# Kernel tuning notes

Measured on AMD Instinct MI355X. Metric: run time of the kernel, lower is better.

## Reference

```python
import jax, jax.numpy as jnp
import numpy as np
from jax import lax

B, T, D = 32, 1024, 512
UNITS, WINDOW = 512, 3


def setup_inputs() -> dict:
    key = jax.random.key(0)
    k1, k2 = jax.random.split(key)
    x = jax.random.normal(k1, (B, T, D), dtype=jnp.float32)
    kernel = jax.random.normal(k2, (WINDOW, D, UNITS * 3), dtype=jnp.float32) * 0.05
    return {"x": x, "kernel": kernel}


def reference(x, kernel):
    units = kernel.shape[2] // 3
    # valid conv1d, channels_last: [B, T, D] x [W, D, 3U] -> [B, T-W+1, 3U]
    conv = lax.conv_general_dilated(
        x, kernel, window_strides=(1,), padding='VALID',
        dimension_numbers=('NWC', 'WIO', 'NWC'))
    Z = conv[..., :units]
    F = conv[..., units:2 * units]
    O = conv[..., 2 * units:]
    z = jnp.tanh(Z)
    f = jax.nn.sigmoid(F)
    o = jax.nn.sigmoid(O)

    # fo-pooling recurrence over time (time-major scan)
    def step(c, zfo):
        z_t, f_t, o_t = zfo
        c_t = f_t * c + (1.0 - f_t) * z_t
        return c_t, o_t * c_t

    c0 = jnp.zeros((x.shape[0], units), dtype=x.dtype)
    zf = (z.transpose(1, 0, 2), f.transpose(1, 0, 2), o.transpose(1, 0, 2))
    _, hs = lax.scan(step, c0, zf)
    return hs.transpose(1, 0, 2)  # [B, T-W+1, units] (ret_sequence=True)
```

## Files before the change

kernel.cpp:

```cpp
#include <hip/hip_runtime.h>
#include <hip/hip_bf16.h>

typedef unsigned short u16;
typedef unsigned short u16x8 __attribute__((ext_vector_type(8)));
typedef short s16x8 __attribute__((ext_vector_type(8)));
typedef float f32x4 __attribute__((ext_vector_type(4)));

#define BATCH 32
#define TPAD 1024
#define TOUT 1022
#define DIM 512
#define KDIM 1536
#define NDIM 1536
#define MPAD (BATCH * TPAD)

#define XB_ELEMS  (MPAD * DIM + 1024)
#define XB_BYTES  (XB_ELEMS * 2)
#define WT_ELEMS  (NDIM * KDIM)
#define WT_BYTES  (WT_ELEMS * 2)
#define ACTS_OFF  (XB_BYTES + WT_BYTES)

__device__ __forceinline__ u16 f2bf(float f) {
    union { __hip_bfloat16 h; u16 u; } v;
    v.h = __float2bfloat16(f);
    return v.u;
}
__device__ __forceinline__ float bf2f(u16 u) {
    union { unsigned int i; float f; } v;
    v.i = ((unsigned int)u) << 16;
    return v.f;
}

__device__ __forceinline__ void gload_lds16(const void* g, void* l) {
    __builtin_amdgcn_global_load_lds(
        (const __attribute__((address_space(1))) void*)g,
        (__attribute__((address_space(3))) void*)l, 16, 0, 0);
}

#define BARRIER() do { asm volatile("" ::: "memory"); \
                       __builtin_amdgcn_s_barrier(); \
                       asm volatile("" ::: "memory"); } while (0)

__global__ __launch_bounds__(256) void cvt_x_kernel(const float* __restrict__ x,
                                                    u16* __restrict__ xb) {
    const int n = MPAD * DIM;
    const int ntot = XB_ELEMS;
    int i = (blockIdx.x * 256 + threadIdx.x) * 8;
    if (i >= ntot) return;
    if (i + 8 <= n) {
        const float4* p = (const float4*)(x + i);
        float4 a = p[0], b = p[1];
        u16x8 r;
        r[0] = f2bf(a.x); r[1] = f2bf(a.y); r[2] = f2bf(a.z); r[3] = f2bf(a.w);
        r[4] = f2bf(b.x); r[5] = f2bf(b.y); r[6] = f2bf(b.z); r[7] = f2bf(b.w);
        *(u16x8*)(xb + i) = r;
    } else {
        for (int q = 0; q < 8 && i + q < ntot; q++)
            xb[i + q] = (i + q < n) ? f2bf(x[i + q]) : (u16)0;
    }
}

__global__ __launch_bounds__(256) void cvt_w_kernel(const float* __restrict__ w,
                                                    u16* __restrict__ wT) {
    __shared__ u16 tile[32][33];
    int tx = threadIdx.x & 31, ty = threadIdx.x >> 5;
    int kt = blockIdx.x * 32, jt = blockIdx.y * 32;
#pragma unroll
    for (int q = 0; q < 4; q++) {
        int k = kt + ty + q * 8;
        tile[ty + q * 8][tx] = f2bf(w[(size_t)k * NDIM + jt + tx]);
    }
    __syncthreads();
#pragma unroll
    for (int q = 0; q < 4; q++) {
        int j = jt + ty + q * 8;
        wT[(size_t)j * KDIM + kt + tx] = tile[tx][ty + q * 8];
    }
}

__global__ __launch_bounds__(512, 2) void gemm_kernel(const u16* __restrict__ xb,
                                                      const u16* __restrict__ wT,
                                                      u16* __restrict__ acts) {
    __shared__ u16 lsA[256 * 64];
    __shared__ u16 lsB[256 * 64];

    const int tid  = threadIdx.x;
    const int lane = tid & 63;
    const int w    = tid >> 6;
    const int wr   = w >> 2;
    const int wc   = w & 3;

    const int wg  = blockIdx.x;
    const int gid = (wg & 7) * 96 + (wg >> 3);
    const int bm  = gid / 6;
    const int bn  = gid % 6;

    const int l15  = lane & 15;
    const int kgrp = (lane >> 4) * 16;
    const int xorv = (lane & 7) << 4;

    const int sc = ((lane & 7) ^ (lane >> 3)) << 4;
    const char* gsrc[8];
    char* ldst[8];
    {
        const char* gA = (const char*)xb;
        const char* gB = (const char*)wT;
#pragma unroll
        for (int g = 0; g < 4; g++) {
            int r0 = wr * 128 + g * 32 + wc * 8;
            int idx = (g < 2) ? g : (4 + g);
            gsrc[idx] = gA + (size_t)(bm * 256 + r0 + (lane >> 3)) * 1024 + sc;
            ldst[idx] = (char*)lsA + r0 * 128;
        }
#pragma unroll
        for (int h = 0; h < 4; h++) {
            int r0 = wc * 64 + h * 16 + wr * 8;
            int idx = 2 + h;
            gsrc[idx] = gB + (size_t)(bn * 256 + r0 + (lane >> 3)) * 3072 + sc;
            ldst[idx] = (char*)lsB + r0 * 128;
        }
    }

    f32x4 acc[8][4] = {};
    s16x8 a[4][2];
    s16x8 b[2][2][2];

#define STAGE(IDX) gload_lds16(gsrc[IDX] + koff, ldst[IDX])

#define LOAD_A(QM) \
    _Pragma("unroll") for (int ii = 0; ii < 4; ii++) \
    _Pragma("unroll") for (int kk = 0; kk < 2; kk++) { \
        int row = wr * 128 + (QM) * 64 + ii * 16 + l15; \
        int byte = (row * 128 + kk * 64 + kgrp) ^ xorv; \
        a[ii][kk] = *(const s16x8*)((const char*)lsA + byte); }

#define LOAD_B(QN) \
    _Pragma("unroll") for (int jj = 0; jj < 2; jj++) \
    _Pragma("unroll") for (int kk = 0; kk < 2; kk++) { \
        int row = wc * 64 + (QN) * 32 + jj * 16 + l15; \
        int byte = (row * 128 + kk * 64 + kgrp) ^ xorv; \
        b[QN][jj][kk] = *(const s16x8*)((const char*)lsB + byte); }

#define MFMA_QUAD(QM, QN) \
    __builtin_amdgcn_s_setprio(1); \
    _Pragma("unroll") for (int ii = 0; ii < 4; ii++) \
    _Pragma("unroll") for (int jj = 0; jj < 2; jj++) \
    _Pragma("unroll") for (int kk = 0; kk < 2; kk++) \
        acc[(QM)*4+ii][(QN)*2+jj] = __builtin_amdgcn_mfma_f32_16x16x32_bf16( \
            a[ii][kk], b[QN][jj][kk], acc[(QM)*4+ii][(QN)*2+jj], 0, 0, 0); \
    __builtin_amdgcn_s_setprio(0);

    {
        size_t koff = 0;
        STAGE(0); STAGE(1); STAGE(2); STAGE(3);
        STAGE(4); STAGE(5); STAGE(6); STAGE(7);
    }

    const int NT = KDIM / 64;
    for (int kt = 0; kt < NT; kt++) {
        const int knext = (kt + 1 == NT) ? 0 : (kt + 1);
        const size_t koff = (size_t)knext * 128;

        asm volatile("s_waitcnt vmcnt(4)" ::: "memory");
        BARRIER();
        LOAD_A(0)
        LOAD_B(0)
        MFMA_QUAD(0, 0)
        BARRIER();

        asm volatile("s_waitcnt vmcnt(2)" ::: "memory");
        BARRIER();
        STAGE(0); STAGE(1); STAGE(2); STAGE(3);
        LOAD_B(1)
        MFMA_QUAD(0, 1)
        BARRIER();

        asm volatile("s_waitcnt vmcnt(4)" ::: "memory");
        BARRIER();
        STAGE(4); STAGE(5);
        LOAD_A(1)
        MFMA_QUAD(1, 1)
        BARRIER();

        STAGE(6); STAGE(7);
        MFMA_QUAD(1, 0)
        BARRIER();
    }

    asm volatile("s_waitcnt vmcnt(0)" ::: "memory");

#undef STAGE
#undef LOAD_A
#undef LOAD_B
#undef MFMA_QUAD

    const int m0 = bm * 256 + wr * 128 + ((lane >> 4) << 2);
    const int n0 = bn * 256 + wc * 64 + (lane & 15);
#pragma unroll
    for (int i = 0; i < 8; i++)
#pragma unroll
        for (int j = 0; j < 4; j++)
#pragma unroll
            for (int r = 0; r < 4; r++) {
                int m = m0 + i * 16 + r;
                int n = n0 + j * 16;
                acts[(size_t)m * NDIM + n] = f2bf(acc[i][j][r]);
            }
}

#define CHUNK 64
__global__ __launch_bounds__(1024) void scan_kernel(const u16* __restrict__ acts,
                                                    float* __restrict__ out) {
    __shared__ float sA[16][64];
    __shared__ float sB[16][64];
    const int lane = threadIdx.x & 63;
    const int w = threadIdx.x >> 6;
    const int b = blockIdx.x >> 3;
    const int u = ((blockIdx.x & 7) << 6) + lane;
    const u16* base = acts + (size_t)b * TPAD * NDIM;
    const int t0 = w * CHUNK;
    const int t1 = (t0 + CHUNK < TOUT) ? (t0 + CHUNK) : TOUT;

    float A = 1.f, Bc = 0.f;
    int t = t0;
    for (; t + 8 <= t1; t += 8) {
        u16 zv[8], fv[8];
#pragma unroll
        for (int q = 0; q < 8; q++) {
            const u16* r = base + (size_t)(t + q) * NDIM;
            zv[q] = r[u]; fv[q] = r[512 + u];
        }
#pragma unroll
        for (int q = 0; q < 8; q++) {
            float z = tanhf(bf2f(zv[q]));
            float f = 1.f / (1.f + __expf(-bf2f(fv[q])));
            Bc = f * Bc + (1.f - f) * z;
            A *= f;
        }
    }
    for (; t < t1; t++) {
        const u16* r = base + (size_t)t * NDIM;
        float z = tanhf(bf2f(r[u]));
        float f = 1.f / (1.f + __expf(-bf2f(r[512 + u])));
        Bc = f * Bc + (1.f - f) * z;
        A *= f;
    }
    sA[w][lane] = A; sB[w][lane] = Bc;
    __syncthreads();

    float c = 0.f;
    for (int w2 = 0; w2 < w; w2++)
        c = sA[w2][lane] * c + sB[w2][lane];

    float* ob = out + (size_t)b * (TOUT * DIM) + u;
    t = t0;
    for (; t + 8 <= t1; t += 8) {
        u16 zv[8], fv[8], ov[8];
#pragma unroll
        for (int q = 0; q < 8; q++) {
            const u16* r = base + (size_t)(t + q) * NDIM;
            zv[q] = r[u]; fv[q] = r[512 + u]; ov[q] = r[1024 + u];
        }
#pragma unroll
        for (int q = 0; q < 8; q++) {
            float z = tanhf(bf2f(zv[q]));
            float f = 1.f / (1.f + __expf(-bf2f(fv[q])));
            float o = 1.f / (1.f + __expf(-bf2f(ov[q])));
            c = f * c + (1.f - f) * z;
            ob[(size_t)(t + q) * DIM] = o * c;
        }
    }
    for (; t < t1; t++) {
        const u16* r = base + (size_t)t * NDIM;
        float z = tanhf(bf2f(r[u]));
        float f = 1.f / (1.f + __expf(-bf2f(r[512 + u])));
        float o = 1.f / (1.f + __expf(-bf2f(r[1024 + u])));
        c = f * c + (1.f - f) * z;
        ob[(size_t)t * DIM] = o * c;
    }
}

extern "C" void kernel_launch(void* const* d_in, const int* in_sizes, int n_in,
                              void* d_out, int out_size, void* d_ws, size_t ws_size,
                              hipStream_t stream) {
    const float* x = (const float*)d_in[0];
    const float* w = (const float*)d_in[1];
    float* out = (float*)d_out;
    char* ws = (char*)d_ws;

    u16* xb   = (u16*)ws;
    u16* wT   = (u16*)(ws + XB_BYTES);
    u16* acts = (u16*)(ws + ACTS_OFF);

    cvt_x_kernel<<<dim3((XB_ELEMS / 8 + 255) / 256), dim3(256), 0, stream>>>(x, xb);
    cvt_w_kernel<<<dim3(KDIM / 32, NDIM / 32), dim3(256), 0, stream>>>(w, wT);
    gemm_kernel<<<dim3(768), dim3(512), 0, stream>>>(xb, wT, acts);
    scan_kernel<<<dim3(256), dim3(1024), 0, stream>>>(acts, out);
}
```

Measured before the change: 236.3 us.

## Software-pipeline LDS fragment loads behind MFMAs with double-buffered registers

The GEMM main loop is restructured so that each quadrant's MFMAs use register fragments loaded in the previous phase, while the next fragments are read from LDS afterwards. A and B fragments get separate register sets (a1/a2, b0/b1v), and the next tile's first fragments are prefetched at the end of each iteration, with fewer barriers per iteration. The intent is to hide LDS read latency behind matrix-core work. In exchange it uses more VGPRs, and the reordered waitcnt and barrier placement carries a risk of LDS read/write races with the in-flight global-to-LDS stages.

```diff
diff --git a/kernel.cpp b/kernel.cpp
--- a/kernel.cpp
+++ b/kernel.cpp
@@ -122,32 +122,34 @@
     }
 
     f32x4 acc[8][4] = {};
-    s16x8 a[4][2];
-    s16x8 b[2][2][2];
+    s16x8 a1[4][2];
+    s16x8 a2[4][2];
+    s16x8 b0[2][2];
+    s16x8 b1v[2][2];
 
 #define STAGE(IDX) gload_lds16(gsrc[IDX] + koff, ldst[IDX])
 
-#define LOAD_A(QM) \
+#define LOAD_A(DST, QM) \
     _Pragma("unroll") for (int ii = 0; ii < 4; ii++) \
     _Pragma("unroll") for (int kk = 0; kk < 2; kk++) { \
         int row = wr * 128 + (QM) * 64 + ii * 16 + l15; \
         int byte = (row * 128 + kk * 64 + kgrp) ^ xorv; \
-        a[ii][kk] = *(const s16x8*)((const char*)lsA + byte); }
-
-#define LOAD_B(QN) \
+        DST[ii][kk] = *(const s16x8*)((const char*)lsA + byte); }
+
+#define LOAD_B(DST, QN) \
     _Pragma("unroll") for (int jj = 0; jj < 2; jj++) \
     _Pragma("unroll") for (int kk = 0; kk < 2; kk++) { \
         int row = wc * 64 + (QN) * 32 + jj * 16 + l15; \
         int byte = (row * 128 + kk * 64 + kgrp) ^ xorv; \
-        b[QN][jj][kk] = *(const s16x8*)((const char*)lsB + byte); }
-
-#define MFMA_QUAD(QM, QN) \
+        DST[jj][kk] = *(const s16x8*)((const char*)lsB + byte); }
+
+#define MFMA_QUAD(ASET, BSET, QM, QN) \
     __builtin_amdgcn_s_setprio(1); \
     _Pragma("unroll") for (int ii = 0; ii < 4; ii++) \
     _Pragma("unroll") for (int jj = 0; jj < 2; jj++) \
     _Pragma("unroll") for (int kk = 0; kk < 2; kk++) \
         acc[(QM)*4+ii][(QN)*2+jj] = __builtin_amdgcn_mfma_f32_16x16x32_bf16( \
-            a[ii][kk], b[QN][jj][kk], acc[(QM)*4+ii][(QN)*2+jj], 0, 0, 0); \
+            ASET[ii][kk], BSET[jj][kk], acc[(QM)*4+ii][(QN)*2+jj], 0, 0, 0); \
     __builtin_amdgcn_s_setprio(0);
 
     {
@@ -155,36 +157,37 @@
         STAGE(0); STAGE(1); STAGE(2); STAGE(3);
         STAGE(4); STAGE(5); STAGE(6); STAGE(7);
     }
+    asm volatile("s_waitcnt vmcnt(4)" ::: "memory");
+    BARRIER();
+    LOAD_A(a1, 0)
+    LOAD_B(b0, 0)
 
     const int NT = KDIM / 64;
     for (int kt = 0; kt < NT; kt++) {
         const int knext = (kt + 1 == NT) ? 0 : (kt + 1);
         const size_t koff = (size_t)knext * 128;
 
-        asm volatile("s_waitcnt vmcnt(4)" ::: "memory");
-        BARRIER();
-        LOAD_A(0)
-        LOAD_B(0)
-        MFMA_QUAD(0, 0)
-        BARRIER();
-
         asm volatile("s_waitcnt vmcnt(2)" ::: "memory");
         BARRIER();
+        MFMA_QUAD(a1, b0, 0, 0)
+        LOAD_B(b1v, 1)
+
+        asm volatile("s_waitcnt vmcnt(0)" ::: "memory");
+        BARRIER();
+        MFMA_QUAD(a1, b1v, 0, 1)
+        LOAD_A(a2, 1)
         STAGE(0); STAGE(1); STAGE(2); STAGE(3);
-        LOAD_B(1)
-        MFMA_QUAD(0, 1)
+
         BARRIER();
-
-        asm volatile("s_waitcnt vmcnt(4)" ::: "memory");
+        MFMA_QUAD(a2, b1v, 1, 1)
+        STAGE(4); STAGE(5);
+
+        asm volatile("s_waitcnt vmcnt(2)" ::: "memory");
         BARRIER();
-        STAGE(4); STAGE(5);
-        LOAD_A(1)
-        MFMA_QUAD(1, 1)
-        BARRIER();
-
+        MFMA_QUAD(a2, b0, 1, 0)
+        LOAD_A(a1, 0)
+        LOAD_B(b0, 0)
         STAGE(6); STAGE(7);
-        MFMA_QUAD(1, 0)
-        BARRIER();
     }
 
     asm volatile("s_waitcnt vmcnt(0)" ::: "memory");
```

Result: faster. 221.7 us (-6.2%).
